# Kernel optimization log

Measured on AMD Instinct MI355X. Metric: run time of the kernel, lower is better.

## Reference

```python
import jax, jax.numpy as jnp
import numpy as np

NUM_EMBED = 204
HEAD_DIM = 64
B, T = 4, 4096


def setup_inputs() -> dict:
    key = jax.random.key(0)
    kx, kq, kk, kv = jax.random.split(key, 4)
    x = jax.random.normal(kx, (B, T, NUM_EMBED), dtype=jnp.float32)
    s = 1.0 / np.sqrt(NUM_EMBED)
    Wq = jax.random.normal(kq, (NUM_EMBED, HEAD_DIM), dtype=jnp.float32) * s
    Wk = jax.random.normal(kk, (NUM_EMBED, HEAD_DIM), dtype=jnp.float32) * s
    Wv = jax.random.normal(kv, (NUM_EMBED, HEAD_DIM), dtype=jnp.float32) * s
    return {"x": x, "Wq": Wq, "Wk": Wk, "Wv": Wv, "mask": True}


def reference(x, Wq, Wk, Wv, mask):
    # Single-head causal attention. d_k = x.shape[-1] (as in the source, which
    # scales by sqrt of the INPUT embed dim, not head_dim).
    Bn, Tn, d_k = x.shape
    q = x @ Wq  # [B,T,H]
    k = x @ Wk  # [B,T,H]
    v = x @ Wv  # [B,T,H]
    scale = 1.0 / jnp.sqrt(jnp.asarray(d_k, dtype=x.dtype))
    scores = jnp.einsum("bqh,bkh->bqk", q, k) * scale  # [B,T,T]
    if mask:
        causal = jnp.tril(jnp.ones((Tn, Tn), dtype=bool))  # allow j <= i
        scores = jnp.where(causal, scores, jnp.finfo(scores.dtype).min)
    attn = jax.nn.softmax(scores, axis=-1)
    out = jnp.einsum("bqk,bkh->bqh", attn, v)  # [B,T,H]
    # dropout is identity in eval mode
    return out
```

## Files before the change

kernel.cpp:

```cpp
#include <hip/hip_runtime.h>

#define TSEQ   4096
#define NB     4
#define EMB    204
#define HD     64
#define WK     224
#define XSTR   232
#define KTILE  64

typedef __attribute__((ext_vector_type(8))) short bf16x8;
typedef __attribute__((ext_vector_type(4))) float f32x4;
typedef __attribute__((ext_vector_type(16))) float f32x16;
typedef __attribute__((ext_vector_type(4))) unsigned u32x4;

__device__ __forceinline__ short f2bf(float f) {
    unsigned u = __float_as_uint(f);
    return (short)((u + 0x7fffu + ((u >> 16) & 1u)) >> 16);
}

__global__ __launch_bounds__(256) void prep_kernel(
    const float* __restrict__ Wq,
    const float* __restrict__ Wk,
    const float* __restrict__ Wv,
    short* __restrict__ Wt)
{
    int f = blockIdx.x * 256 + threadIdx.x;
    if (f < 3 * HD * WK) {
        int e   = f % WK;
        int h   = (f / WK) % HD;
        int mat = f / (WK * HD);
        const float* W = (mat == 0) ? Wq : (mat == 1) ? Wk : Wv;
        float v = (e < EMB) ? W[e * HD + h] : 0.f;
        Wt[f] = f2bf(v);
    }
}

__global__ __launch_bounds__(192) void qkv_mfma_kernel(
    const float* __restrict__ x,
    const short* __restrict__ Wt,
    short* __restrict__ qg,
    short* __restrict__ kg,
    short* __restrict__ vtg)
{
    __shared__ __align__(16) short xs[16 * XSTR];

    const int t    = threadIdx.x;
    const int lane = t & 63;
    const int w    = t >> 6;
    const int l15  = lane & 15;
    const int quad = lane >> 4;
    const long long rowb = (long long)blockIdx.x * 16;

    for (int c = t; c < 816; c += 192) {
        int r = c / 51, c4 = c % 51;
        float4 xv = *(const float4*)(x + (rowb + r) * EMB + c4 * 4);
        unsigned p0 = (unsigned)(unsigned short)f2bf(xv.x)
                    | ((unsigned)(unsigned short)f2bf(xv.y) << 16);
        unsigned p1 = (unsigned)(unsigned short)f2bf(xv.z)
                    | ((unsigned)(unsigned short)f2bf(xv.w) << 16);
        uint2 pk; pk.x = p0; pk.y = p1;
        *(uint2*)(&xs[r * XSTR + c4 * 4]) = pk;
    }
    for (int c = t; c < 16 * 28; c += 192) {
        int r = c / 28, cc = c % 28;
        xs[r * XSTR + EMB + cc] = 0;
    }
    __syncthreads();

    f32x4 acc[4];
#pragma unroll
    for (int nt = 0; nt < 4; ++nt) acc[nt] = (f32x4){0.f, 0.f, 0.f, 0.f};

    const short* Wb = Wt + (size_t)w * HD * WK;
#pragma unroll
    for (int ks = 0; ks < 7; ++ks) {
        bf16x8 af = *(const bf16x8*)(&xs[l15 * XSTR + ks * 32 + quad * 8]);
#pragma unroll
        for (int nt = 0; nt < 4; ++nt) {
            bf16x8 bfr = *(const bf16x8*)(Wb + (size_t)(nt * 16 + l15) * WK
                                          + ks * 32 + quad * 8);
            acc[nt] = __builtin_amdgcn_mfma_f32_16x16x32_bf16(af, bfr, acc[nt], 0, 0, 0);
        }
    }

    const float scale = 0.101008857f;
    if (w == 0) {
#pragma unroll
        for (int r = 0; r < 4; ++r) {
            long long grow = rowb + quad * 4 + r;
#pragma unroll
            for (int nt = 0; nt < 4; ++nt)
                qg[grow * HD + nt * 16 + l15] = f2bf(acc[nt][r] * scale);
        }
    } else if (w == 1) {
#pragma unroll
        for (int r = 0; r < 4; ++r) {
            long long grow = rowb + quad * 4 + r;
#pragma unroll
            for (int nt = 0; nt < 4; ++nt)
                kg[grow * HD + nt * 16 + l15] = f2bf(acc[nt][r]);
        }
    } else {
#pragma unroll
        for (int r = 0; r < 4; ++r) {
            long long grow = rowb + quad * 4 + r;
            int bb = (int)(grow >> 12);
            int tt = (int)(grow & 4095);
#pragma unroll
            for (int nt = 0; nt < 4; ++nt)
                vtg[((long long)bb * HD + nt * 16 + l15) * TSEQ + tt] = f2bf(acc[nt][r]);
        }
    }
}

__global__ __launch_bounds__(256, 4) void flash_mfma_kernel(
    const short* __restrict__ qg,
    const short* __restrict__ kg,
    const short* __restrict__ vtg,
    float* __restrict__ oparts,
    float* __restrict__ lparts,
    int NSEGk, int smax)
{
    __shared__ __align__(16) short Ks[2][KTILE * HD];
    __shared__ __align__(16) short Vt[2][HD * KTILE];

    const int t    = threadIdx.x;
    const int lane = t & 63;
    const int w    = t >> 6;
    const int l31  = lane & 31;
    const int hi   = lane >> 5;
    const int wq   = w * 32;

    const int b = blockIdx.y;
    const int p = NSEGk - 1 - (int)blockIdx.x;

    int qt3 = 0, base = 0;
    for (;; ++qt3) {
        int sg = (qt3 + 2) >> 1;
        if (sg > smax) sg = smax;
        if (p < base + sg) break;
        base += sg;
    }
    int s = (qt3 + 2) >> 1;
    if (s > smax) s = smax;
    const int split  = p - base;
    const int ntiles = 2 * qt3 + 2;
    const int chunk  = (ntiles + s - 1) / s;
    const int kt0    = split * chunk;
    const int kt1    = min(ntiles, kt0 + chunk);

    const int qbase = qt3 * 128;
    const long long rowb = (long long)b * TSEQ;
    const int qA = qbase + wq + l31;

    bf16x8 aq[4];
#pragma unroll
    for (int c = 0; c < 4; ++c)
        aq[c] = *(const bf16x8*)(qg + (rowb + qA) * HD + c * 16 + hi * 8);

    f32x16 Oacc[2];
#pragma unroll
    for (int hg = 0; hg < 2; ++hg)
#pragma unroll
        for (int r = 0; r < 16; ++r) Oacc[hg][r] = 0.f;
    float lsum = 0.f;

#define STAGE(BUF, KT) do {                                                   \
        const int k0s = (KT) * KTILE;                                         \
        _Pragma("unroll")                                                     \
        for (int j = 0; j < 2; ++j) {                                         \
            const int rr = (w * 2 + j) * 8 + (lane >> 3);                     \
            const int cc = (lane & 7) ^ (rr & 7);                             \
            const short* srcK = kg + (rowb + k0s + rr) * HD + cc * 8;         \
            __builtin_amdgcn_global_load_lds(                                 \
                (const __attribute__((address_space(1))) void*)srcK,          \
                (__attribute__((address_space(3))) void*)&Ks[BUF][(w * 2 + j) * 512], \
                16, 0, 0);                                                    \
            const short* srcV = vtg + ((long long)b * HD + rr) * TSEQ + k0s + cc * 8; \
            __builtin_amdgcn_global_load_lds(                                 \
                (const __attribute__((address_space(1))) void*)srcV,          \
                (__attribute__((address_space(3))) void*)&Vt[BUF][(w * 2 + j) * 512], \
                16, 0, 0);                                                    \
        }                                                                     \
    } while (0)

    int cur = 0;
    STAGE(0, kt0);
    __syncthreads();

    for (int kt = kt0; kt < kt1; ++kt) {
        const int k0 = kt * KTILE;
        if (kt + 1 < kt1) STAGE(cur ^ 1, kt + 1);

        const short* ksb = Ks[cur];
        const short* vsb = Vt[cur];
        const bool act  = (k0 <= qbase + wq + 31);
        const bool full = (k0 + 63 <= qbase + wq);

        if (act) {
            unsigned cd[2][8];
#pragma unroll
            for (int kg2 = 0; kg2 < 2; ++kg2) {
                f32x16 S;
#pragma unroll
                for (int r = 0; r < 16; ++r) S[r] = 0.f;
#pragma unroll
                for (int c = 0; c < 4; ++c) {
                    bf16x8 kf = *(const bf16x8*)(ksb + (kg2 * 32 + l31) * HD
                                   + (((2 * c + hi) ^ (l31 & 7)) * 8));
                    S = __builtin_amdgcn_mfma_f32_32x32x16_bf16(kf, aq[c], S, 0, 0, 0);
                }
                const int jb = k0 + kg2 * 32 + 4 * hi;
#pragma unroll
                for (int g = 0; g < 8; ++g) {
                    float e0 = __builtin_amdgcn_exp2f(S[2 * g]);
                    float e1 = __builtin_amdgcn_exp2f(S[2 * g + 1]);
                    if (!full) {
                        const int j0 = jb + 8 * (g >> 1) + 2 * (g & 1);
                        if (j0     > qA) e0 = 0.f;
                        if (j0 + 1 > qA) e1 = 0.f;
                    }
                    lsum += e0 + e1;
                    asm("v_cvt_pk_bf16_f32 %0, %1, %2"
                        : "=v"(cd[kg2][g]) : "v"(e0), "v"(e1));
                }
            }

#pragma unroll
            for (int kc = 0; kc < 4; ++kc) {
                unsigned u0 = cd[kc >> 1][4 * (kc & 1) + 0];
                unsigned u1 = cd[kc >> 1][4 * (kc & 1) + 1];
                unsigned u2 = cd[kc >> 1][4 * (kc & 1) + 2];
                unsigned u3 = cd[kc >> 1][4 * (kc & 1) + 3];
                asm("v_permlane32_swap_b32 %0, %1" : "+v"(u0), "+v"(u2));
                asm("v_permlane32_swap_b32 %0, %1" : "+v"(u1), "+v"(u3));
                u32x4 pk = {u0, u1, u2, u3};
                bf16x8 pb = __builtin_bit_cast(bf16x8, pk);
#pragma unroll
                for (int hg = 0; hg < 2; ++hg) {
                    bf16x8 vf = *(const bf16x8*)(vsb + (hg * 32 + l31) * HD
                                   + (((2 * kc + hi) ^ (l31 & 7)) * 8));
                    Oacc[hg] = __builtin_amdgcn_mfma_f32_32x32x16_bf16(vf, pb, Oacc[hg], 0, 0, 0);
                }
            }
        }

        __syncthreads();
        cur ^= 1;
    }

    float* optr = oparts + ((size_t)b * NSEGk + p) * 8192
                + (size_t)w * 2048 + (size_t)lane * 32;
#pragma unroll
    for (int hg = 0; hg < 2; ++hg)
#pragma unroll
        for (int rq = 0; rq < 4; ++rq) {
            float4 v = make_float4(Oacc[hg][4 * rq + 0], Oacc[hg][4 * rq + 1],
                                   Oacc[hg][4 * rq + 2], Oacc[hg][4 * rq + 3]);
            *(float4*)(optr + hg * 16 + rq * 4) = v;
        }

    lsum += __shfl_xor(lsum, 32, 64);
    if (hi == 0)
        lparts[((size_t)b * NSEGk + p) * 128 + w * 32 + l31] = lsum;
#undef STAGE
}

__global__ __launch_bounds__(256) void finalize_kernel(
    const float* __restrict__ oparts,
    const float* __restrict__ lparts,
    float* __restrict__ out,
    int NSEGk, int smax)
{
    const int row = blockIdx.x * 16 + (threadIdx.x >> 4);
    const int c0  = (threadIdx.x & 15) * 4;
    const int b = row >> 12, rowin = row & 4095;
    const int qt3 = rowin >> 7, w = (rowin >> 5) & 3, l31 = rowin & 31;

    int segbase = 0;
    for (int j = 0; j < qt3; ++j) {
        int sg = (j + 2) >> 1;
        if (sg > smax) sg = smax;
        segbase += sg;
    }
    int s = (qt3 + 2) >> 1;
    if (s > smax) s = smax;

    const int hg = c0 >> 5, hiq = (c0 >> 2) & 1, rq = (c0 & 31) >> 3;
    const int lane = hiq * 32 + l31;

    const float* obase = oparts + ((size_t)b * NSEGk + segbase) * 8192
                       + (size_t)w * 2048 + (size_t)lane * 32 + hg * 16 + rq * 4;
    const float* lbase = lparts + ((size_t)b * NSEGk + segbase) * 128 + w * 32 + l31;

    float4 acc = make_float4(0.f, 0.f, 0.f, 0.f);
    float lsum = 0.f;
    for (int k = 0; k < s; ++k) {
        float4 v = *(const float4*)(obase + (size_t)k * 8192);
        acc.x += v.x; acc.y += v.y; acc.z += v.z; acc.w += v.w;
        lsum += lbase[(size_t)k * 128];
    }
    float inv = 1.0f / lsum;
    acc.x *= inv; acc.y *= inv; acc.z *= inv; acc.w *= inv;
    *(float4*)(out + (size_t)row * HD + c0) = acc;
}

extern "C" void kernel_launch(void* const* d_in, const int* in_sizes, int n_in,
                              void* d_out, int out_size, void* d_ws, size_t ws_size,
                              hipStream_t stream)
{
    const float* x  = (const float*)d_in[0];
    const float* Wq = (const float*)d_in[1];
    const float* Wk = (const float*)d_in[2];
    const float* Wv = (const float*)d_in[3];

    const size_t nrows = (size_t)NB * TSEQ;

    const size_t fixed_bytes = 3 * nrows * HD * 2 + (size_t)3 * HD * WK * 2;
    int smax = 1, NSEG = 32;
    const int cands[3] = {8, 4, 2};
    for (int i = 0; i < 3; ++i) {
        int sm = cands[i], ns = 0;
        for (int q = 0; q < 32; ++q) {
            int sg = (q + 2) >> 1;
            if (sg > sm) sg = sm;
            ns += sg;
        }
        size_t need = fixed_bytes + (size_t)NB * ns * (8192 + 128) * 4;
        if (need <= ws_size) { smax = sm; NSEG = ns; break; }
    }

    short* qg  = (short*)d_ws;
    short* kg  = qg + nrows * HD;
    short* vtg = kg + nrows * HD;
    short* Wt  = vtg + nrows * HD;
    float* oparts = (float*)(Wt + 3 * HD * WK);
    float* lparts = oparts + (size_t)NB * NSEG * 8192;
    float* outp = (float*)d_out;

    prep_kernel<<<dim3(168), dim3(256), 0, stream>>>(Wq, Wk, Wv, Wt);
    qkv_mfma_kernel<<<dim3(1024), dim3(192), 0, stream>>>(x, Wt, qg, kg, vtg);
    flash_mfma_kernel<<<dim3(NSEG, NB), dim3(256), 0, stream>>>(qg, kg, vtg,
                                                               oparts, lparts,
                                                               NSEG, smax);
    finalize_kernel<<<dim3(1024), dim3(256), 0, stream>>>(oparts, lparts, outp,
                                                          NSEG, smax);
}
```

Baseline: 109.9 us.

## Fuse split-K reduction into flash kernel via atomic last-block finalize

Removes the separate finalize kernel. Each split-K attention block now bumps a per-query-tile atomic counter, and the last block to finish reduces all partials and writes the normalized output. Splits are now a fixed number of key tiles per segment (6) rather than a capped count, and single-segment tiles write the output directly. Launch bounds go to 5 waves/SIMD. This saves a kernel launch and some partial traffic, but adds threadfence/atomic serialization and a tail reduction done by one block per tile.

Measured after the change: 294.4 us. 168% more time.

```diff
diff --git a/kernel.cpp b/kernel.cpp
--- a/kernel.cpp
+++ b/kernel.cpp
@@ -22,7 +22,8 @@
     const float* __restrict__ Wq,
     const float* __restrict__ Wk,
     const float* __restrict__ Wv,
-    short* __restrict__ Wt)
+    short* __restrict__ Wt,
+    int* __restrict__ flags)
 {
     int f = blockIdx.x * 256 + threadIdx.x;
     if (f < 3 * HD * WK) {
@@ -33,6 +34,8 @@
         float v = (e < EMB) ? W[e * HD + h] : 0.f;
         Wt[f] = f2bf(v);
     }
+    if (blockIdx.x == 0 && threadIdx.x < NB * 32)
+        flags[threadIdx.x] = 0;
 }
 
 __global__ __launch_bounds__(192) void qkv_mfma_kernel(
@@ -113,13 +116,15 @@
     }
 }
 
-__global__ __launch_bounds__(256, 4) void flash_mfma_kernel(
+__global__ __launch_bounds__(256, 5) void flash_mfma_kernel(
     const short* __restrict__ qg,
     const short* __restrict__ kg,
     const short* __restrict__ vtg,
     float* __restrict__ oparts,
     float* __restrict__ lparts,
-    int NSEGk, int smax)
+    float* __restrict__ out,
+    int* __restrict__ flags,
+    int NSEGk, int CH)
 {
     __shared__ __align__(16) short Ks[2][KTILE * HD];
     __shared__ __align__(16) short Vt[2][HD * KTILE];
@@ -134,20 +139,16 @@
     const int b = blockIdx.y;
     const int p = NSEGk - 1 - (int)blockIdx.x;
 
-    int qt3 = 0, base = 0;
+    int qt3 = 0, base = 0, s = 1;
     for (;; ++qt3) {
-        int sg = (qt3 + 2) >> 1;
-        if (sg > smax) sg = smax;
-        if (p < base + sg) break;
-        base += sg;
-    }
-    int s = (qt3 + 2) >> 1;
-    if (s > smax) s = smax;
+        s = (2 * qt3 + 2 + CH - 1) / CH;
+        if (p < base + s) break;
+        base += s;
+    }
     const int split  = p - base;
     const int ntiles = 2 * qt3 + 2;
-    const int chunk  = (ntiles + s - 1) / s;
-    const int kt0    = split * chunk;
-    const int kt1    = min(ntiles, kt0 + chunk);
+    const int kt0    = split * CH;
+    const int kt1    = min(ntiles, kt0 + CH);
 
     const int qbase = qt3 * 128;
     const long long rowb = (long long)b * TSEQ;
@@ -249,6 +250,24 @@
         cur ^= 1;
     }
 
+    lsum += __shfl_xor(lsum, 32, 64);
+
+    if (s == 1) {
+        const float inv = 1.0f / lsum;
+        float* orow = out + (rowb + qA) * HD;
+#pragma unroll
+        for (int hg = 0; hg < 2; ++hg)
+#pragma unroll
+            for (int rq = 0; rq < 4; ++rq) {
+                float4 v = make_float4(Oacc[hg][4 * rq + 0] * inv,
+                                       Oacc[hg][4 * rq + 1] * inv,
+                                       Oacc[hg][4 * rq + 2] * inv,
+                                       Oacc[hg][4 * rq + 3] * inv);
+                *(float4*)(orow + hg * 32 + hi * 4 + rq * 8) = v;
+            }
+        return;
+    }
+
     float* optr = oparts + ((size_t)b * NSEGk + p) * 8192
                 + (size_t)w * 2048 + (size_t)lane * 32;
 #pragma unroll
@@ -259,50 +278,48 @@
                                    Oacc[hg][4 * rq + 2], Oacc[hg][4 * rq + 3]);
             *(float4*)(optr + hg * 16 + rq * 4) = v;
         }
-
-    lsum += __shfl_xor(lsum, 32, 64);
     if (hi == 0)
         lparts[((size_t)b * NSEGk + p) * 128 + w * 32 + l31] = lsum;
+
+    __threadfence();
+    __syncthreads();
+    volatile int* donep = (volatile int*)&Ks[0][0];
+    if (t == 0) {
+        int old = atomicAdd(&flags[b * 32 + qt3], 1);
+        *donep = (old == s - 1) ? 1 : 0;
+    }
+    __syncthreads();
+    if (*donep == 0) return;
+
+    __threadfence();
+    const float* osegs = oparts + ((size_t)b * NSEGk + base) * 8192;
+    const float* lsegs = lparts + ((size_t)b * NSEGk + base) * 128;
+
+    float* linv = (float*)&Vt[0][0];
+    if (t < 128) {
+        float a = 0.f;
+        for (int k = 0; k < s; ++k) a += lsegs[(size_t)k * 128 + t];
+        linv[t] = 1.0f / a;
+    }
+    __syncthreads();
+
+    for (int i = t * 4; i < 8192; i += 1024) {
+        float4 a = *(const float4*)(osegs + i);
+        for (int k = 1; k < s; ++k) {
+            float4 v = *(const float4*)(osegs + (size_t)k * 8192 + i);
+            a.x += v.x; a.y += v.y; a.z += v.z; a.w += v.w;
+        }
+        const int wseg  = i >> 11;
+        const int lane2 = (i >> 5) & 63;
+        const int hg2   = (i >> 4) & 1;
+        const int rq2   = (i >> 2) & 3;
+        const int lrow  = wseg * 32 + (lane2 & 31);
+        const float inv = linv[lrow];
+        a.x *= inv; a.y *= inv; a.z *= inv; a.w *= inv;
+        const int col = hg2 * 32 + (lane2 >> 5) * 4 + rq2 * 8;
+        *(float4*)(out + (rowb + qbase + lrow) * HD + col) = a;
+    }
 #undef STAGE
-}
-
-__global__ __launch_bounds__(256) void finalize_kernel(
-    const float* __restrict__ oparts,
-    const float* __restrict__ lparts,
-    float* __restrict__ out,
-    int NSEGk, int smax)
-{
-    const int row = blockIdx.x * 16 + (threadIdx.x >> 4);
-    const int c0  = (threadIdx.x & 15) * 4;
-    const int b = row >> 12, rowin = row & 4095;
-    const int qt3 = rowin >> 7, w = (rowin >> 5) & 3, l31 = rowin & 31;
-
-    int segbase = 0;
-    for (int j = 0; j < qt3; ++j) {
-        int sg = (j + 2) >> 1;
-        if (sg > smax) sg = smax;
-        segbase += sg;
-    }
-    int s = (qt3 + 2) >> 1;
-    if (s > smax) s = smax;
-
-    const int hg = c0 >> 5, hiq = (c0 >> 2) & 1, rq = (c0 & 31) >> 3;
-    const int lane = hiq * 32 + l31;
-
-    const float* obase = oparts + ((size_t)b * NSEGk + segbase) * 8192
-                       + (size_t)w * 2048 + (size_t)lane * 32 + hg * 16 + rq * 4;
-    const float* lbase = lparts + ((size_t)b * NSEGk + segbase) * 128 + w * 32 + l31;
-
-    float4 acc = make_float4(0.f, 0.f, 0.f, 0.f);
-    float lsum = 0.f;
-    for (int k = 0; k < s; ++k) {
-        float4 v = *(const float4*)(obase + (size_t)k * 8192);
-        acc.x += v.x; acc.y += v.y; acc.z += v.z; acc.w += v.w;
-        lsum += lbase[(size_t)k * 128];
-    }
-    float inv = 1.0f / lsum;
-    acc.x *= inv; acc.y *= inv; acc.z *= inv; acc.w *= inv;
-    *(float4*)(out + (size_t)row * HD + c0) = acc;
 }
 
 extern "C" void kernel_launch(void* const* d_in, const int* in_sizes, int n_in,
@@ -316,19 +333,12 @@
 
     const size_t nrows = (size_t)NB * TSEQ;
 
+    int CH = 6, NSEG = 0;
+    for (int q = 0; q < 32; ++q) NSEG += (2 * q + 2 + CH - 1) / CH;
     const size_t fixed_bytes = 3 * nrows * HD * 2 + (size_t)3 * HD * WK * 2;
-    int smax = 1, NSEG = 32;
-    const int cands[3] = {8, 4, 2};
-    for (int i = 0; i < 3; ++i) {
-        int sm = cands[i], ns = 0;
-        for (int q = 0; q < 32; ++q) {
-            int sg = (q + 2) >> 1;
-            if (sg > sm) sg = sm;
-            ns += sg;
-        }
-        size_t need = fixed_bytes + (size_t)NB * ns * (8192 + 128) * 4;
-        if (need <= ws_size) { smax = sm; NSEG = ns; break; }
-    }
+    size_t need = fixed_bytes + (size_t)NB * NSEG * (8192 + 128) * 4
+                + (size_t)NB * 32 * 4;
+    if (need > ws_size) { CH = 64; NSEG = 32; }
 
     short* qg  = (short*)d_ws;
     short* kg  = qg + nrows * HD;
@@ -336,13 +346,13 @@
     short* Wt  = vtg + nrows * HD;
     float* oparts = (float*)(Wt + 3 * HD * WK);
     float* lparts = oparts + (size_t)NB * NSEG * 8192;
+    int*   flags  = (int*)(lparts + (size_t)NB * NSEG * 128);
     float* outp = (float*)d_out;
 
-    prep_kernel<<<dim3(168), dim3(256), 0, stream>>>(Wq, Wk, Wv, Wt);
+    prep_kernel<<<dim3(168), dim3(256), 0, stream>>>(Wq, Wk, Wv, Wt, flags);
     qkv_mfma_kernel<<<dim3(1024), dim3(192), 0, stream>>>(x, Wt, qg, kg, vtg);
     flash_mfma_kernel<<<dim3(NSEG, NB), dim3(256), 0, stream>>>(qg, kg, vtg,
                                                                oparts, lparts,
-                                                               NSEG, smax);
-    finalize_kernel<<<dim3(1024), dim3(256), 0, stream>>>(oparts, lparts, outp,
-                                                          NSEG, smax);
-}
+                                                               outp, flags,
+                                                               NSEG, CH);
+}
```
